# Optimization experiments

Measured on AMD Instinct MI355X. Metric: run time of the kernel, lower is better.

Reference implementation:

```python
import jax, jax.numpy as jnp
import numpy as np

FOUR_PI = 4.0 * np.pi
INF_CLAMP = 1e30


def setup_inputs() -> dict:
    key = jax.random.key(0)
    k1, k2, k3, k4 = jax.random.split(key, 4)
    B, N, M, S = 16, 2048, 16, 128
    pcl_transformed = jax.random.normal(k1, (B, N, M, 3), dtype=jnp.float32)
    primitive_points = jax.random.normal(k2, (B, M, S, 3), dtype=jnp.float32)
    size = jax.random.uniform(k3, (B, M, 3), dtype=jnp.float32, minval=0.05, maxval=1.0)
    probs = jax.random.uniform(k4, (B, M), dtype=jnp.float32)
    return {"pcl_transformed": pcl_transformed, "primitive_points": primitive_points,
            "size": size, "probs": probs}


def reference(pcl_transformed, primitive_points, size, probs):
    B, N, M, _ = pcl_transformed.shape
    S = primitive_points.shape[2]

    # diff: (B, M, S, N, 3); dist: (B, M, S, N)
    diff = primitive_points[:, :, :, None, :] - jnp.transpose(pcl_transformed, (0, 2, 1, 3))[:, :, None, :, :]
    dist = jnp.sum(diff * diff, axis=-1)

    # ---- pcl_to_prim loss (min over S, sort over M, stick-breaking cumprod) ----
    d1 = jnp.transpose(jnp.min(dist, axis=2), (0, 2, 1))  # (B, N, M)
    idx = jnp.argsort(d1, axis=-1)                         # (B, N, M)
    distance = jnp.take_along_axis(d1, idx, axis=-1)
    p = jnp.take_along_axis(jnp.broadcast_to(probs[:, None, :], (B, N, M)), idx, axis=-1)
    neg_cumprod = jnp.cumprod(1.0 - p, axis=-1)
    neg_cumprod = jnp.concatenate([jnp.ones_like(neg_cumprod[..., :1]), neg_cumprod[..., :-1]], axis=-1)
    minprob = p * neg_cumprod
    pcl_to_prim = jnp.einsum('bnm,bnm->', distance, minprob) / (B * N)

    # ---- prim_to_pcl loss (min over N, superquadric-area weighting) ----
    d2 = jnp.min(dist, axis=-1)                            # (B, M, S)
    d2 = jnp.where(d2 >= INF_CLAMP, 0.0, d2)
    s0, s1, s2 = size[..., 0], size[..., 1], size[..., 2]
    area = FOUR_PI * ((s0 * s1) ** 1.6 / 3 + (s0 * s2) ** 1.6 / 3 + (s1 * s2) ** 1.6 / 3) ** 0.625
    area = M * area / jnp.sum(area, axis=-1, keepdims=True)  # (B, M)
    prim_to_pcl = jnp.einsum('bm,bm,bm->', jnp.mean(d2, axis=-1), probs, area) / (B * M)

    # No regularizer types enabled -> regs == 0 (matches regularizer_type=[]).
    regs = jnp.zeros((), dtype=pcl_to_prim.dtype)
    total = 1.0 * pcl_to_prim + 1.0 * prim_to_pcl + regs
    return total, pcl_to_prim, prim_to_pcl, regs
```

## Files before the change

kernel.cpp:

```cpp
#include <hip/hip_runtime.h>
#include <math.h>

#define BB 16
#define NN 2048
#define MM 16
#define SS 128

__constant__ const float kFourPi = 12.566370614359172f;

__global__ __launch_bounds__(256) void prep_kernel(
    const float* __restrict__ pcl,
    const float* __restrict__ prim,
    float4* __restrict__ PclP,
    float4* __restrict__ PrimP,
    unsigned int* __restrict__ counter)
{
    const int b   = blockIdx.x;
    const int tid = threadIdx.x;

    if (blockIdx.x == 0 && blockIdx.y == 0 && tid == 0)
        __hip_atomic_store(counter, 0u, __ATOMIC_RELAXED, __HIP_MEMORY_SCOPE_AGENT);

    if (blockIdx.y < 16) {
        const int n0 = blockIdx.y * 128;
        __shared__ float q[6144];
        const float4* src = (const float4*)(pcl + ((size_t)b * NN + n0) * (MM * 3));
        float4* qv = (float4*)q;
#pragma unroll
        for (int k = 0; k < 6; ++k)
            qv[tid + k * 256] = src[tid + k * 256];
        __syncthreads();

        const int n  = tid & 127;
        const int mh = tid >> 7;
#pragma unroll
        for (int k = 0; k < 8; ++k) {
            const int m = k * 2 + mh;
            const float x = q[(n * 16 + m) * 3 + 0];
            const float y = q[(n * 16 + m) * 3 + 1];
            const float z = q[(n * 16 + m) * 3 + 2];
            const float h = 0.5f * (x * x + y * y + z * z);
            PclP[((size_t)(b * MM + m)) * NN + n0 + n] = make_float4(x, y, z, h);
        }
    } else {
        const float* pp = prim + (size_t)b * (MM * SS * 3);
#pragma unroll
        for (int k = 0; k < 8; ++k) {
            const int p = tid + k * 256;
            const float x = pp[p * 3 + 0];
            const float y = pp[p * 3 + 1];
            const float z = pp[p * 3 + 2];
            const float h = 0.5f * (x * x + y * y + z * z);
            PrimP[(size_t)b * (MM * SS) + p] = make_float4(x, y, z, h);
        }
    }
}

__global__ __launch_bounds__(256, 4) void dist3_kernel(
    const float4* __restrict__ PclP,
    const float4* __restrict__ PrimP,
    float* __restrict__ d1part,
    float* __restrict__ d2part)
{
    const int bm  = blockIdx.x;
    const int cs  = blockIdx.y;
    const int tid = threadIdx.x;
    const int wid  = tid >> 6;
    const int lane = tid & 63;

    __shared__ float4 Plds[32];
    __shared__ float  wred[4][64];

    if (tid < 32)
        Plds[tid] = PrimP[(size_t)bm * SS + cs * 32 + tid];

    float qx[8], qy[8], qz[8], hq[8], d1m[8];
    const float4* qp = PclP + (size_t)bm * NN + tid;
#pragma unroll
    for (int j = 0; j < 8; ++j) {
        const float4 q = qp[j * 256];
        qx[j] = q.x; qy[j] = q.y; qz[j] = q.z; hq[j] = q.w;
        d1m[j] = 3.0e38f;
    }
    __syncthreads();

    float d2r[32];
#pragma unroll
    for (int s = 0; s < 32; ++s) {
        const float4 f = Plds[s];
        float e[8];
#pragma unroll
        for (int j = 0; j < 8; ++j) {
            float t = hq[j] + f.w;
            t = fmaf(f.x, -qx[j], t);
            t = fmaf(f.y, -qy[j], t);
            t = fmaf(f.z, -qz[j], t);
            e[j] = t;
            d1m[j] = fminf(d1m[j], t);
        }
        const float m01 = fminf(e[0], e[1]);
        const float m23 = fminf(e[2], e[3]);
        const float m45 = fminf(e[4], e[5]);
        const float m67 = fminf(e[6], e[7]);
        d2r[s] = fminf(fminf(m01, m23), fminf(m45, m67));
    }

    float* dd = d1part + ((size_t)(cs * 256 + bm)) * NN + tid;
#pragma unroll
    for (int j = 0; j < 8; ++j) dd[j * 256] = d1m[j];

    float v16[16];
    {
        const bool hi = (lane & 32) != 0;
#pragma unroll
        for (int k = 0; k < 16; ++k) {
            const float xk = hi ? d2r[k + 16] : d2r[k];
            const float xs = hi ? d2r[k] : d2r[k + 16];
            v16[k] = fminf(xk, __shfl_xor(xs, 32, 64));
        }
    }
    float v8[8];
    {
        const bool hi = (lane & 16) != 0;
#pragma unroll
        for (int k = 0; k < 8; ++k) {
            const float xk = hi ? v16[k + 8] : v16[k];
            const float xs = hi ? v16[k] : v16[k + 8];
            v8[k] = fminf(xk, __shfl_xor(xs, 16, 64));
        }
    }
    float v4[4];
    {
        const bool hi = (lane & 8) != 0;
#pragma unroll
        for (int k = 0; k < 4; ++k) {
            const float xk = hi ? v8[k + 4] : v8[k];
            const float xs = hi ? v8[k] : v8[k + 4];
            v4[k] = fminf(xk, __shfl_xor(xs, 8, 64));
        }
    }
    float v2[2];
    {
        const bool hi = (lane & 4) != 0;
        const float xk0 = hi ? v4[2] : v4[0];
        const float xs0 = hi ? v4[0] : v4[2];
        v2[0] = fminf(xk0, __shfl_xor(xs0, 4, 64));
        const float xk1 = hi ? v4[3] : v4[1];
        const float xs1 = hi ? v4[1] : v4[3];
        v2[1] = fminf(xk1, __shfl_xor(xs1, 4, 64));
    }
    float v1;
    {
        const bool hi = (lane & 2) != 0;
        const float xk = hi ? v2[1] : v2[0];
        const float xs = hi ? v2[0] : v2[1];
        v1 = fminf(xk, __shfl_xor(xs, 2, 64));
    }
    const float r = fminf(v1, __shfl_xor(v1, 1, 64));
    wred[wid][lane] = r;
    __syncthreads();

    if (tid < 64) {
        float mv = fminf(fminf(wred[0][tid], wred[1][tid]),
                         fminf(wred[2][tid], wred[3][tid]));
        if (mv >= 5.0e29f) mv = 0.0f;
#pragma unroll
        for (int off = 32; off > 0; off >>= 1)
            mv += __shfl_down(mv, off, 64);
        if (tid == 0) d2part[cs * 256 + bm] = mv;
    }
}

__global__ __launch_bounds__(256) void p2p_final_kernel(
    const float* __restrict__ d1part,
    const float* __restrict__ probs,
    const float* __restrict__ size_,
    const float* __restrict__ d2part,
    float* __restrict__ partial,
    unsigned int* __restrict__ counter,
    float* __restrict__ out)
{
    const int tid = threadIdx.x;
    const int gid = blockIdx.x * 256 + tid;
    const int b   = gid >> 11;
    const int n   = gid & (NN - 1);

    float d[16], p[16];
#pragma unroll
    for (int m = 0; m < 16; ++m) {
        const size_t base = ((size_t)(b * MM + m)) * NN + n;
        const float v0 = d1part[base];
        const float v1 = d1part[base + (size_t)256 * NN];
        const float v2 = d1part[base + (size_t)512 * NN];
        const float v3 = d1part[base + (size_t)768 * NN];
        const float mn = fminf(fminf(v0, v1), fminf(v2, v3));
        d[m] = mn + mn;
    }

    const float* pb = probs + b * MM;
#pragma unroll
    for (int k = 0; k < 16; ++k) p[k] = pb[k];

#define CE(i, j)                                              \
    {                                                         \
        const bool c = d[i] > d[j];                           \
        const float td = c ? d[j] : d[i];                     \
        d[j] = c ? d[i] : d[j];  d[i] = td;                   \
        const float tp = c ? p[j] : p[i];                     \
        p[j] = c ? p[i] : p[j];  p[i] = tp;                   \
    }
#pragma unroll
    for (int r = 0; r < 16; ++r) {
        if ((r & 1) == 0) {
            CE(0, 1) CE(2, 3) CE(4, 5) CE(6, 7)
            CE(8, 9) CE(10, 11) CE(12, 13) CE(14, 15)
        } else {
            CE(1, 2) CE(3, 4) CE(5, 6) CE(7, 8)
            CE(9, 10) CE(11, 12) CE(13, 14)
        }
    }
#undef CE

    float acc = 1.0f, sum = 0.0f;
#pragma unroll
    for (int k = 0; k < 16; ++k) {
        sum += d[k] * p[k] * acc;
        acc *= (1.0f - p[k]);
    }

    const int wid  = tid >> 6;
    const int lane = tid & 63;
    __shared__ float red4[4];
#pragma unroll
    for (int off = 32; off > 0; off >>= 1)
        sum += __shfl_down(sum, off, 64);
    if (lane == 0) red4[wid] = sum;
    __syncthreads();

    __shared__ bool amLast;
    if (tid == 0) {
        const float bsum = red4[0] + red4[1] + red4[2] + red4[3];
        __hip_atomic_store(&partial[blockIdx.x], bsum,
                           __ATOMIC_RELEASE, __HIP_MEMORY_SCOPE_AGENT);
        const unsigned int prev = __hip_atomic_fetch_add(
            counter, 1u, __ATOMIC_ACQ_REL, __HIP_MEMORY_SCOPE_AGENT);
        amLast = (prev == 127u);
    }
    __syncthreads();
    if (!amLast) return;

    const int fb = tid >> 4;

    __shared__ float  areaSh[256];
    __shared__ double redA[4];
    __shared__ double redB[4];

    const float s0 = size_[tid * 3 + 0];
    const float s1 = size_[tid * 3 + 1];
    const float s2 = size_[tid * 3 + 2];
    const float inner = powf(s0 * s1, 1.6f) * (1.0f / 3.0f)
                      + powf(s0 * s2, 1.6f) * (1.0f / 3.0f)
                      + powf(s1 * s2, 1.6f) * (1.0f / 3.0f);
    const float a = kFourPi * powf(inner, 0.625f);
    areaSh[tid] = a;
    __syncthreads();

    float asum = 0.0f;
#pragma unroll
    for (int mm = 0; mm < 16; ++mm) asum += areaSh[fb * 16 + mm];
    const float anorm = 16.0f * a / asum;

    const float d2s = d2part[tid] + d2part[256 + tid] + d2part[512 + tid] + d2part[768 + tid];
    double t = (double)(d2s * (1.0f / 128.0f)) * (double)probs[tid] * (double)anorm;
#pragma unroll
    for (int off = 32; off > 0; off >>= 1)
        t += __shfl_down(t, off, 64);
    if (lane == 0) redA[wid] = t;

    double u = 0.0;
    if (tid < 128) {
        const float pv = __hip_atomic_load(&partial[tid],
                                           __ATOMIC_ACQUIRE, __HIP_MEMORY_SCOPE_AGENT);
        u = (double)pv;
    }
#pragma unroll
    for (int off = 32; off > 0; off >>= 1)
        u += __shfl_down(u, off, 64);
    if (lane == 0) redB[wid] = u;

    __syncthreads();
    if (tid == 0) {
        const double prim_to_pcl = (redA[0] + redA[1] + redA[2] + redA[3]) / 256.0;
        const double pcl_to_prim = (redB[0] + redB[1] + redB[2] + redB[3]) / 32768.0;
        out[0] = (float)(pcl_to_prim + prim_to_pcl);
        out[1] = (float)pcl_to_prim;
        out[2] = (float)prim_to_pcl;
        out[3] = 0.0f;
    }
}


extern "C" void kernel_launch(void* const* d_in, const int* in_sizes, int n_in,
                              void* d_out, int out_size, void* d_ws, size_t ws_size,
                              hipStream_t stream) {
    const float* pcl   = (const float*)d_in[0];
    const float* prim  = (const float*)d_in[1];
    const float* size_ = (const float*)d_in[2];
    const float* probs = (const float*)d_in[3];
    float* out = (float*)d_out;

    const size_t nBMN = (size_t)BB * MM * NN;
    float4* PclP  = (float4*)d_ws;
    float4* PrimP = PclP + nBMN;
    float*  d1part = (float*)(PrimP + (size_t)BB * MM * SS);
    float*  d2part = d1part + 4 * nBMN;
    float*  partial = d2part + 1024;
    unsigned int* counter = (unsigned int*)(partial + 128);

    prep_kernel<<<dim3(BB, 17), 256, 0, stream>>>(pcl, prim, PclP, PrimP, counter);
    dist3_kernel<<<dim3(BB * MM, 4), 256, 0, stream>>>(PclP, PrimP, d1part, d2part);
    p2p_final_kernel<<<128, 256, 0, stream>>>(d1part, probs, size_, d2part, partial, counter, out);
}
```

Measured before the change: 90.31 us.

## Fuse distance and final reduction kernels with per-batch spin-wait flags

```diff
diff --git a/kernel.cpp b/kernel.cpp
--- a/kernel.cpp
+++ b/kernel.cpp
@@ -13,13 +13,13 @@
     const float* __restrict__ prim,
     float4* __restrict__ PclP,
     float4* __restrict__ PrimP,
-    unsigned int* __restrict__ counter)
+    unsigned int* __restrict__ flags)
 {
     const int b   = blockIdx.x;
     const int tid = threadIdx.x;
 
-    if (blockIdx.x == 0 && blockIdx.y == 0 && tid == 0)
-        __hip_atomic_store(counter, 0u, __ATOMIC_RELAXED, __HIP_MEMORY_SCOPE_AGENT);
+    if (blockIdx.x == 0 && blockIdx.y == 0 && tid < 17)
+        __hip_atomic_store(&flags[tid], 0u, __ATOMIC_RELAXED, __HIP_MEMORY_SCOPE_AGENT);
 
     if (blockIdx.y < 16) {
         const int n0 = blockIdx.y * 128;
@@ -56,14 +56,21 @@
     }
 }
 
-__global__ __launch_bounds__(256, 4) void dist3_kernel(
+__global__ __launch_bounds__(256, 4) void mega_kernel(
     const float4* __restrict__ PclP,
     const float4* __restrict__ PrimP,
     float* __restrict__ d1part,
-    float* __restrict__ d2part)
+    float* __restrict__ d2part,
+    const float* __restrict__ probs,
+    const float* __restrict__ size_,
+    float* __restrict__ partial,
+    unsigned int* __restrict__ flags,
+    float* __restrict__ out)
 {
-    const int bm  = blockIdx.x;
-    const int cs  = blockIdx.y;
+    const int id  = blockIdx.x;
+    const int bm  = id >> 2;
+    const int cs  = id & 3;
+    const int b   = bm >> 4;
     const int tid = threadIdx.x;
     const int wid  = tid >> 6;
     const int lane = tid & 63;
@@ -105,9 +112,11 @@
         d2r[s] = fminf(fminf(m01, m23), fminf(m45, m67));
     }
 
-    float* dd = d1part + ((size_t)(cs * 256 + bm)) * NN + tid;
-#pragma unroll
-    for (int j = 0; j < 8; ++j) dd[j * 256] = d1m[j];
+    {
+        float* dd = d1part + ((size_t)(cs * 256 + bm)) * NN + tid;
+#pragma unroll
+        for (int j = 0; j < 8; ++j) dd[j * 256] = d1m[j];
+    }
 
     float v16[16];
     {
@@ -139,21 +148,21 @@
             v4[k] = fminf(xk, __shfl_xor(xs, 8, 64));
         }
     }
-    float v2[2];
+    float v2a, v2b;
     {
         const bool hi = (lane & 4) != 0;
         const float xk0 = hi ? v4[2] : v4[0];
         const float xs0 = hi ? v4[0] : v4[2];
-        v2[0] = fminf(xk0, __shfl_xor(xs0, 4, 64));
+        v2a = fminf(xk0, __shfl_xor(xs0, 4, 64));
         const float xk1 = hi ? v4[3] : v4[1];
         const float xs1 = hi ? v4[1] : v4[3];
-        v2[1] = fminf(xk1, __shfl_xor(xs1, 4, 64));
+        v2b = fminf(xk1, __shfl_xor(xs1, 4, 64));
     }
     float v1;
     {
         const bool hi = (lane & 2) != 0;
-        const float xk = hi ? v2[1] : v2[0];
-        const float xs = hi ? v2[0] : v2[1];
+        const float xk = hi ? v2b : v2a;
+        const float xs = hi ? v2a : v2b;
         v1 = fminf(xk, __shfl_xor(xs, 2, 64));
     }
     const float r = fminf(v1, __shfl_xor(v1, 1, 64));
@@ -169,35 +178,34 @@
             mv += __shfl_down(mv, off, 64);
         if (tid == 0) d2part[cs * 256 + bm] = mv;
     }
-}
-
-__global__ __launch_bounds__(256) void p2p_final_kernel(
-    const float* __restrict__ d1part,
-    const float* __restrict__ probs,
-    const float* __restrict__ size_,
-    const float* __restrict__ d2part,
-    float* __restrict__ partial,
-    unsigned int* __restrict__ counter,
-    float* __restrict__ out)
-{
-    const int tid = threadIdx.x;
-    const int gid = blockIdx.x * 256 + tid;
-    const int b   = gid >> 11;
+
+    __threadfence();
+    __syncthreads();
+    if (tid == 0)
+        __hip_atomic_fetch_add(&flags[b], 1u, __ATOMIC_RELEASE, __HIP_MEMORY_SCOPE_AGENT);
+
+    if (id >= 128) return;
+
+    const int wb = id >> 3;
+    while (__hip_atomic_load(&flags[wb], __ATOMIC_ACQUIRE, __HIP_MEMORY_SCOPE_AGENT) < 64u)
+        __builtin_amdgcn_s_sleep(2);
+
+    const int gid = id * 256 + tid;
     const int n   = gid & (NN - 1);
 
     float d[16], p[16];
 #pragma unroll
     for (int m = 0; m < 16; ++m) {
-        const size_t base = ((size_t)(b * MM + m)) * NN + n;
-        const float v0 = d1part[base];
-        const float v1 = d1part[base + (size_t)256 * NN];
-        const float v2 = d1part[base + (size_t)512 * NN];
-        const float v3 = d1part[base + (size_t)768 * NN];
-        const float mn = fminf(fminf(v0, v1), fminf(v2, v3));
+        const size_t base = ((size_t)(wb * MM + m)) * NN + n;
+        const float u0 = d1part[base];
+        const float u1 = d1part[base + (size_t)256 * NN];
+        const float u2 = d1part[base + (size_t)512 * NN];
+        const float u3 = d1part[base + (size_t)768 * NN];
+        const float mn = fminf(fminf(u0, u1), fminf(u2, u3));
         d[m] = mn + mn;
     }
 
-    const float* pb = probs + b * MM;
+    const float* pb = probs + wb * MM;
 #pragma unroll
     for (int k = 0; k < 16; ++k) p[k] = pb[k];
 
@@ -210,8 +218,8 @@
         p[j] = c ? p[i] : p[j];  p[i] = tp;                   \
     }
 #pragma unroll
-    for (int r = 0; r < 16; ++r) {
-        if ((r & 1) == 0) {
+    for (int rr = 0; rr < 16; ++rr) {
+        if ((rr & 1) == 0) {
             CE(0, 1) CE(2, 3) CE(4, 5) CE(6, 7)
             CE(8, 9) CE(10, 11) CE(12, 13) CE(14, 15)
         } else {
@@ -228,8 +236,6 @@
         acc *= (1.0f - p[k]);
     }
 
-    const int wid  = tid >> 6;
-    const int lane = tid & 63;
     __shared__ float red4[4];
 #pragma unroll
     for (int off = 32; off > 0; off >>= 1)
@@ -240,10 +246,10 @@
     __shared__ bool amLast;
     if (tid == 0) {
         const float bsum = red4[0] + red4[1] + red4[2] + red4[3];
-        __hip_atomic_store(&partial[blockIdx.x], bsum,
+        __hip_atomic_store(&partial[id], bsum,
                            __ATOMIC_RELEASE, __HIP_MEMORY_SCOPE_AGENT);
         const unsigned int prev = __hip_atomic_fetch_add(
-            counter, 1u, __ATOMIC_ACQ_REL, __HIP_MEMORY_SCOPE_AGENT);
+            &flags[16], 1u, __ATOMIC_ACQ_REL, __HIP_MEMORY_SCOPE_AGENT);
         amLast = (prev == 127u);
     }
     __syncthreads();
@@ -310,14 +316,14 @@
     float* out = (float*)d_out;
 
     const size_t nBMN = (size_t)BB * MM * NN;
-    float4* PclP  = (float4*)d_ws;
-    float4* PrimP = PclP + nBMN;
+    float4* PclP   = (float4*)d_ws;
+    float4* PrimP  = PclP + nBMN;
     float*  d1part = (float*)(PrimP + (size_t)BB * MM * SS);
     float*  d2part = d1part + 4 * nBMN;
     float*  partial = d2part + 1024;
-    unsigned int* counter = (unsigned int*)(partial + 128);
-
-    prep_kernel<<<dim3(BB, 17), 256, 0, stream>>>(pcl, prim, PclP, PrimP, counter);
-    dist3_kernel<<<dim3(BB * MM, 4), 256, 0, stream>>>(PclP, PrimP, d1part, d2part);
-    p2p_final_kernel<<<128, 256, 0, stream>>>(d1part, probs, size_, d2part, partial, counter, out);
+    unsigned int* flags = (unsigned int*)(partial + 128);
+
+    prep_kernel<<<dim3(BB, 17), 256, 0, stream>>>(pcl, prim, PclP, PrimP, flags);
+    mega_kernel<<<1024, 256, 0, stream>>>(PclP, PrimP, d1part, d2part,
+                                          probs, size_, partial, flags, out);
 }
```

Result: slower. 208.8 us (+131.2%).
